# Kernel tuning notes

Measured on AMD Instinct MI355X. Metric: run time of the kernel, lower is better.

The kernel has to match this reference:

```python
import jax, jax.numpy as jnp
import numpy as np

NUM_FIELDS = 32
BATCH = 16384
EMBED_DIM = 64

# static pair index lists, exactly as built in __init__
_pairs = np.array([(i, j) for i in range(NUM_FIELDS - 1) for j in range(i + 1, NUM_FIELDS)], dtype=np.int32)
ROW = jnp.asarray(_pairs[:, 0])  # [P] with P = F*(F-1)/2 = 496
COL = jnp.asarray(_pairs[:, 1])


def setup_inputs() -> dict:
    key = jax.random.key(0)
    x = jax.random.normal(key, (BATCH, NUM_FIELDS, EMBED_DIM), dtype=jnp.float32)
    return {"x": x}


def reference(x):
    # Original: pq[b,k] = sum_{a,b'} p[b,k,a] * q[b,k,b']  (full outer product summed)
    # which is algebraically identical to sum_a(p) * sum_b(q).
    s = jnp.sum(x, axis=-1)          # [B, F]
    return s[:, ROW] * s[:, COL]      # [B, P]
```

## Files before the change

kernel.cpp:

```cpp
#include <hip/hip_runtime.h>

#define NUM_FIELDS 32
#define EMBED_DIM  64
#define NUM_PAIRS  496
#define ROWS       8
#define P4         (NUM_PAIRS / 4)

typedef float f4 __attribute__((ext_vector_type(4)));

struct Pairs {
    unsigned char r[NUM_PAIRS];
    unsigned char c[NUM_PAIRS];
};
constexpr Pairs make_pairs() {
    Pairs t{};
    int p = 0;
    for (int i = 0; i < NUM_FIELDS - 1; ++i)
        for (int j = i + 1; j < NUM_FIELDS; ++j) {
            t.r[p] = (unsigned char)i;
            t.c[p] = (unsigned char)j;
            ++p;
        }
    return t;
}
__device__ constexpr Pairs PAIRS = make_pairs();

__global__ __launch_bounds__(256)
void opn_kernel(const float* __restrict__ x, float* __restrict__ out, int batch) {
    const int t = threadIdx.x;
    const int row0 = blockIdx.x * ROWS;
    if (row0 >= batch) return;

    __shared__ float s_sh[ROWS][NUM_FIELDS];

    const f4* __restrict__ x4 =
        (const f4*)(x + (size_t)row0 * NUM_FIELDS * EMBED_DIM);

    f4 a[ROWS], c[ROWS];
    #pragma unroll
    for (int r = 0; r < ROWS; ++r) {
        a[r] = __builtin_nontemporal_load(&x4[r * 512 + t]);
        c[r] = __builtin_nontemporal_load(&x4[r * 512 + 256 + t]);
    }

    #pragma unroll
    for (int r = 0; r < ROWS; ++r) {
        float p1 = (a[r].x + a[r].y) + (a[r].z + a[r].w);
        float p2 = (c[r].x + c[r].y) + (c[r].z + c[r].w);
        #pragma unroll
        for (int off = 8; off >= 1; off >>= 1) {
            p1 += __shfl_xor(p1, off);
            p2 += __shfl_xor(p2, off);
        }
        if ((t & 15) == 0) {
            const int f = t >> 4;
            s_sh[r][f]      = p1;
            s_sh[r][16 + f] = p2;
        }
    }
    __syncthreads();

    f4* __restrict__ o4 = (f4*)(out + (size_t)row0 * NUM_PAIRS);
    #pragma unroll
    for (int i = t; i < ROWS * P4; i += 256) {
        const int r  = i / P4;
        const int p0 = (i - r * P4) * 4;
        f4 v;
        v.x = s_sh[r][PAIRS.r[p0 + 0]] * s_sh[r][PAIRS.c[p0 + 0]];
        v.y = s_sh[r][PAIRS.r[p0 + 1]] * s_sh[r][PAIRS.c[p0 + 1]];
        v.z = s_sh[r][PAIRS.r[p0 + 2]] * s_sh[r][PAIRS.c[p0 + 2]];
        v.w = s_sh[r][PAIRS.r[p0 + 3]] * s_sh[r][PAIRS.c[p0 + 3]];
        __builtin_nontemporal_store(v, &o4[i]);
    }
}

extern "C" void kernel_launch(void* const* d_in, const int* in_sizes, int n_in,
                              void* d_out, int out_size, void* d_ws, size_t ws_size,
                              hipStream_t stream) {
    const float* x = (const float*)d_in[0];
    float* out = (float*)d_out;
    const int batch = in_sizes[0] / (NUM_FIELDS * EMBED_DIM);
    const int grid = (batch + ROWS - 1) / ROWS;
    opn_kernel<<<grid, 256, 0, stream>>>(x, out, batch);
}
```

Baseline: 189.3 us.

## Assign one batch row per wavefront and drop block-wide barrier

Restructures the kernel so each 64-lane wavefront owns a whole batch row. It loads the row's 8 vector chunks, reduces them with shuffles, writes the 32 field sums to its own shared slice, and computes the 496 products itself. This removes the __syncthreads and the cross-row index division, and uses 512-thread blocks. It relies on wave-level ordering between the shared-memory writes and reads without an explicit fence, and leaves some lanes idle in the second output pass.

```diff
diff --git a/kernel.cpp b/kernel.cpp
--- a/kernel.cpp
+++ b/kernel.cpp
@@ -3,8 +3,8 @@
 #define NUM_FIELDS 32
 #define EMBED_DIM  64
 #define NUM_PAIRS  496
-#define ROWS       8
 #define P4         (NUM_PAIRS / 4)
+#define WAVES      8
 
 typedef float f4 __attribute__((ext_vector_type(4)));
 
@@ -25,52 +25,55 @@
 }
 __device__ constexpr Pairs PAIRS = make_pairs();
 
-__global__ __launch_bounds__(256)
+__global__ __launch_bounds__(WAVES * 64)
 void opn_kernel(const float* __restrict__ x, float* __restrict__ out, int batch) {
-    const int t = threadIdx.x;
-    const int row0 = blockIdx.x * ROWS;
-    if (row0 >= batch) return;
+    const int wave = threadIdx.x >> 6;
+    const int lane = threadIdx.x & 63;
+    const int row  = blockIdx.x * WAVES + wave;
+    if (row >= batch) return;
 
-    __shared__ float s_sh[ROWS][NUM_FIELDS];
+    __shared__ float s_sh[WAVES][NUM_FIELDS];
 
     const f4* __restrict__ x4 =
-        (const f4*)(x + (size_t)row0 * NUM_FIELDS * EMBED_DIM);
+        (const f4*)(x + (size_t)row * NUM_FIELDS * EMBED_DIM);
 
-    f4 a[ROWS], c[ROWS];
+    f4 v[8];
     #pragma unroll
-    for (int r = 0; r < ROWS; ++r) {
-        a[r] = __builtin_nontemporal_load(&x4[r * 512 + t]);
-        c[r] = __builtin_nontemporal_load(&x4[r * 512 + 256 + t]);
+    for (int k = 0; k < 8; ++k)
+        v[k] = __builtin_nontemporal_load(&x4[k * 64 + lane]);
+
+    float p[8];
+    #pragma unroll
+    for (int k = 0; k < 8; ++k)
+        p[k] = (v[k].x + v[k].y) + (v[k].z + v[k].w);
+
+    #pragma unroll
+    for (int off = 8; off >= 1; off >>= 1) {
+        #pragma unroll
+        for (int k = 0; k < 8; ++k)
+            p[k] += __shfl_xor(p[k], off);
     }
 
+    const int g = lane >> 4;
+    if ((lane & 15) == 0) {
+        #pragma unroll
+        for (int k = 0; k < 8; ++k)
+            s_sh[wave][4 * k + g] = p[k];
+    }
+
+    f4* __restrict__ o4 = (f4*)(out + (size_t)row * NUM_PAIRS);
     #pragma unroll
-    for (int r = 0; r < ROWS; ++r) {
-        float p1 = (a[r].x + a[r].y) + (a[r].z + a[r].w);
-        float p2 = (c[r].x + c[r].y) + (c[r].z + c[r].w);
-        #pragma unroll
-        for (int off = 8; off >= 1; off >>= 1) {
-            p1 += __shfl_xor(p1, off);
-            p2 += __shfl_xor(p2, off);
+    for (int rep = 0; rep < 2; ++rep) {
+        const int i = rep * 64 + lane;
+        if (i < P4) {
+            const int p0 = i * 4;
+            f4 r;
+            r.x = s_sh[wave][PAIRS.r[p0 + 0]] * s_sh[wave][PAIRS.c[p0 + 0]];
+            r.y = s_sh[wave][PAIRS.r[p0 + 1]] * s_sh[wave][PAIRS.c[p0 + 1]];
+            r.z = s_sh[wave][PAIRS.r[p0 + 2]] * s_sh[wave][PAIRS.c[p0 + 2]];
+            r.w = s_sh[wave][PAIRS.r[p0 + 3]] * s_sh[wave][PAIRS.c[p0 + 3]];
+            __builtin_nontemporal_store(r, &o4[i]);
         }
-        if ((t & 15) == 0) {
-            const int f = t >> 4;
-            s_sh[r][f]      = p1;
-            s_sh[r][16 + f] = p2;
-        }
-    }
-    __syncthreads();
-
-    f4* __restrict__ o4 = (f4*)(out + (size_t)row0 * NUM_PAIRS);
-    #pragma unroll
-    for (int i = t; i < ROWS * P4; i += 256) {
-        const int r  = i / P4;
-        const int p0 = (i - r * P4) * 4;
-        f4 v;
-        v.x = s_sh[r][PAIRS.r[p0 + 0]] * s_sh[r][PAIRS.c[p0 + 0]];
-        v.y = s_sh[r][PAIRS.r[p0 + 1]] * s_sh[r][PAIRS.c[p0 + 1]];
-        v.z = s_sh[r][PAIRS.r[p0 + 2]] * s_sh[r][PAIRS.c[p0 + 2]];
-        v.w = s_sh[r][PAIRS.r[p0 + 3]] * s_sh[r][PAIRS.c[p0 + 3]];
-        __builtin_nontemporal_store(v, &o4[i]);
     }
 }
 
@@ -80,6 +83,6 @@
     const float* x = (const float*)d_in[0];
     float* out = (float*)d_out;
     const int batch = in_sizes[0] / (NUM_FIELDS * EMBED_DIM);
-    const int grid = (batch + ROWS - 1) / ROWS;
-    opn_kernel<<<grid, 256, 0, stream>>>(x, out, batch);
+    const int grid = (batch + WAVES - 1) / WAVES;
+    opn_kernel<<<grid, WAVES * 64, 0, stream>>>(x, out, batch);
 }
```

Result: no change. 188.3 us (-0.5%).
